# Kernel optimization log

Measured on AMD Instinct MI355X. Metric: run time of the kernel, lower is better.

Reference implementation:

```python
import jax, jax.numpy as jnp
import numpy as np

N, D_IN, H, D_EMB = 2048, 128, 256, 64


def setup_inputs() -> dict:
    key = jax.random.key(0)
    ks = jax.random.split(key, 8)
    x = jax.random.normal(ks[0], (N, D_IN), dtype=jnp.float32)
    adj = jnp.zeros((N, N), dtype=jnp.float32)  # only its last dim is used (eye sizing)
    s = 0.05
    W0 = jax.random.normal(ks[1], (D_IN, H), dtype=jnp.float32) * s
    b0 = jnp.zeros((H,), dtype=jnp.float32)
    W1 = jax.random.normal(ks[2], (H, D_EMB), dtype=jnp.float32) * s
    b1 = jnp.zeros((D_EMB,), dtype=jnp.float32)
    W2 = jax.random.normal(ks[3], (D_IN, D_IN), dtype=jnp.float32) * s
    b2 = jnp.zeros((D_IN,), dtype=jnp.float32)
    temp = jnp.float32(0.1)
    theta = jnp.float32(0.1)
    return {"x": x, "adj": adj, "W0": W0, "b0": b0, "W1": W1, "b1": b1,
            "W2": W2, "b2": b2, "temp": temp, "theta": theta}


def reference(x, adj, W0, b0, W1, b1, W2, b2, temp, theta):
    # layer 0 (on x) and middle layer 1 (on out_x), both with ReLU activation
    out_x = jax.nn.relu(x @ W0 + b0)            # [N, H]
    emb = jax.nn.relu(out_x @ W1 + b1)          # [N, D_EMB]
    # last layer is applied to the ORIGINAL x (per the `x = model(x)` branch)
    x_last = x @ W2 + b2                        # [N, D_IN]

    # dist[i,j] = -||emb_i - emb_j||^2, computed via the gemm expansion
    sq = jnp.sum(emb * emb, axis=1)             # [N]
    dist = -(sq[:, None] + sq[None, :] - 2.0 * (emb @ emb.T))  # [N, N]

    prob = jax.nn.sigmoid((1.0 + temp) * dist + (5.0 + theta))
    A = prob + jnp.eye(adj.shape[-1], dtype=prob.dtype)        # [N, N]

    # diag(A.sum(-1))^{-1} @ A @ x_last  ==  rowwise divide by degree
    deg = jnp.sum(A, axis=-1)                   # [N]
    out = jax.nn.relu((A @ x_last) / deg[:, None])

    # sigmoid(.) > 0 everywhere, so all N*N entries are nonzero: adj_wts is the
    # full flattened adjacency (data-independent shape, jit-safe)
    adj_wts = A.reshape(-1)
    return out, adj_wts
```

## Files before the change

### kernel.cpp

```cpp
#include <hip/hip_runtime.h>
#include <hip/hip_bf16.h>


typedef short bf16x8 __attribute__((ext_vector_type(8)));
typedef float f32x4 __attribute__((ext_vector_type(4)));

__device__ __forceinline__ unsigned short f2bf(float f) {
    unsigned u = __float_as_uint(f);
    unsigned r = u + 0x7fffu + ((u >> 16) & 1u);
    return (unsigned short)(r >> 16);
}

__device__ __forceinline__ bf16x8 pack_bf8(const float* p) {
    union { unsigned u[4]; bf16x8 v; } r;
    #pragma unroll
    for (int i = 0; i < 4; ++i)
        r.u[i] = __builtin_amdgcn_perm(__float_as_uint(p[2 * i + 1]),
                                       __float_as_uint(p[2 * i]), 0x07060302u);
    return r.v;
}

__global__ __launch_bounds__(512) void k1_mlp(
    const float* __restrict__ x,
    const float* __restrict__ W0, const float* __restrict__ b0,
    const float* __restrict__ W1, const float* __restrict__ b1,
    const float* __restrict__ W2, const float* __restrict__ b2,
    unsigned short* __restrict__ emb_bf,
    unsigned short* __restrict__ xlT_bf,
    float* __restrict__ sq,
    float* __restrict__ deg,
    float* __restrict__ outAcc)
{
    __shared__ float xs[8 * 132];
    __shared__ float oxs[8 * 260];
    __shared__ unsigned short xls[128 * 8];
    const int t = threadIdx.x;
    const int r0 = blockIdx.x * 8;

    if (t < 256) {
        int row = t >> 5, c4 = t & 31;
        float4 v = *(const float4*)(x + (r0 + row) * 128 + c4 * 4);
        *(float4*)(&xs[row * 132 + c4 * 4]) = v;
    }
    if (t < 8) deg[r0 + t] = 0.0f;
    *(float2*)(&outAcc[blockIdx.x * 1024 + t * 2]) = make_float2(0.f, 0.f);
    __syncthreads();

    {
        int c = t & 255, rg = t >> 8;
        float bb = b0[c];
        float acc[4] = {bb, bb, bb, bb};
        for (int kk = 0; kk < 32; ++kk) {
            float wa = W0[(kk * 4 + 0) * 256 + c];
            float wb = W0[(kk * 4 + 1) * 256 + c];
            float wc = W0[(kk * 4 + 2) * 256 + c];
            float wd = W0[(kk * 4 + 3) * 256 + c];
            #pragma unroll
            for (int r = 0; r < 4; ++r) {
                float4 xv = *(const float4*)(&xs[(rg * 4 + r) * 132 + kk * 4]);
                acc[r] += xv.x * wa + xv.y * wb + xv.z * wc + xv.w * wd;
            }
        }
        #pragma unroll
        for (int r = 0; r < 4; ++r) oxs[(rg * 4 + r) * 260 + c] = fmaxf(acc[r], 0.0f);
    }
    __syncthreads();

    {
        int h = t & 63, r = t >> 6;
        float acc = b1[h];
        for (int kk = 0; kk < 64; ++kk) {
            float wa = W1[(kk * 4 + 0) * 64 + h];
            float wb = W1[(kk * 4 + 1) * 64 + h];
            float wc = W1[(kk * 4 + 2) * 64 + h];
            float wd = W1[(kk * 4 + 3) * 64 + h];
            float4 xv = *(const float4*)(&oxs[r * 260 + kk * 4]);
            acc += xv.x * wa + xv.y * wb + xv.z * wc + xv.w * wd;
        }
        float e = fmaxf(acc, 0.0f);
        emb_bf[(r0 + r) * 64 + h] = f2bf(e);
        float s = e * e;
        #pragma unroll
        for (int off = 32; off; off >>= 1) s += __shfl_xor(s, off);
        if (h == 0) sq[r0 + r] = s;
    }

    {
        int c = t & 127, rg = t >> 7;
        float bb = b2[c];
        float acc[2] = {bb, bb};
        for (int kk = 0; kk < 32; ++kk) {
            float wa = W2[(kk * 4 + 0) * 128 + c];
            float wb = W2[(kk * 4 + 1) * 128 + c];
            float wc = W2[(kk * 4 + 2) * 128 + c];
            float wd = W2[(kk * 4 + 3) * 128 + c];
            #pragma unroll
            for (int r = 0; r < 2; ++r) {
                float4 xv = *(const float4*)(&xs[(rg * 2 + r) * 132 + kk * 4]);
                acc[r] += xv.x * wa + xv.y * wb + xv.z * wc + xv.w * wd;
            }
        }
        unsigned short p0 = f2bf(acc[0]), p1 = f2bf(acc[1]);
        *(unsigned int*)(&xls[c * 8 + rg * 2]) = (unsigned)p0 | ((unsigned)p1 << 16);
    }
    __syncthreads();
    if (t < 128) {
        uint4 v = *(const uint4*)(&xls[t * 8]);
        *(uint4*)(&xlT_bf[t * 2048 + r0]) = v;
    }
}

__global__ __launch_bounds__(256) void k2f(
    const unsigned short* __restrict__ emb_bf,
    const unsigned short* __restrict__ xlT_bf,
    const float* __restrict__ sq,
    const float* __restrict__ tempp, const float* __restrict__ thetap,
    float* __restrict__ adjw,
    float* __restrict__ outAcc,
    float* __restrict__ deg)
{
    constexpr int LDP = 132;
    __shared__ float Pt[2][16 * LDP];

    const int t = threadIdx.x;
    const int lane = t & 63;
    const int w = t >> 6;
    const int m = lane & 15;
    const int q = lane >> 4;
    const int i0 = blockIdx.x * 16;
    const int jstrip0 = blockIdx.y * 256;
    const float scale = 1.0f + tempp[0];
    const float bias = 5.0f + thetap[0];

    bf16x8 a0 = *(const bf16x8*)(emb_bf + (size_t)(i0 + m) * 64 + q * 8);
    bf16x8 a1 = *(const bf16x8*)(emb_bf + (size_t)(i0 + m) * 64 + 32 + q * 8);
    float sqIr[4];
    #pragma unroll
    for (int r = 0; r < 4; ++r) sqIr[r] = sq[i0 + q * 4 + r];

    f32x4 accO0 = {0.f, 0.f, 0.f, 0.f};
    f32x4 accO1 = {0.f, 0.f, 0.f, 0.f};
    float dega[4] = {0.f, 0.f, 0.f, 0.f};
    const int cg = w * 32;

    #pragma unroll
    for (int jt = 0; jt < 2; ++jt) {
        const int j0 = jstrip0 + jt * 128;
        float* P = &Pt[jt][0];

        #pragma unroll
        for (int s = 0; s < 2; ++s) {
            const int col = (w * 2 + s) * 16 + m;
            const unsigned short* ebj = emb_bf + (size_t)(j0 + col) * 64;
            bf16x8 b0 = *(const bf16x8*)(ebj + q * 8);
            bf16x8 b1 = *(const bf16x8*)(ebj + 32 + q * 8);
            f32x4 S = {0.f, 0.f, 0.f, 0.f};
            S = __builtin_amdgcn_mfma_f32_16x16x32_bf16(a0, b0, S, 0, 0, 0);
            S = __builtin_amdgcn_mfma_f32_16x16x32_bf16(a1, b1, S, 0, 0, 0);

            const float csqJ = sq[j0 + col];
            const int gcol = j0 + col;
            #pragma unroll
            for (int r = 0; r < 4; ++r) {
                int grow = i0 + q * 4 + r;
                float dist = 2.0f * S[r] - sqIr[r] - csqJ;
                float z = scale * dist + bias;
                float p = 1.0f / (1.0f + __expf(-z));
                if (grow == gcol) p += 1.0f;
                dega[r] += p;
                P[(q * 4 + r) * LDP + col] = p;
            }
        }
        __syncthreads();

        {
            int row = t >> 4;
            int c0 = (t & 15) * 8;
            f32x4 v0 = *(const f32x4*)(&P[row * LDP + c0]);
            f32x4 v1 = *(const f32x4*)(&P[row * LDP + c0 + 4]);
            f32x4* dst = (f32x4*)(adjw + (size_t)(i0 + row) * 2048 + j0 + c0);
            __builtin_nontemporal_store(v0, dst);
            __builtin_nontemporal_store(v1, dst + 1);
        }

        #pragma unroll
        for (int s = 0; s < 4; ++s) {
            float af[8];
            *(f32x4*)(&af[0]) = *(const f32x4*)(&P[m * LDP + s * 32 + q * 8]);
            *(f32x4*)(&af[4]) = *(const f32x4*)(&P[m * LDP + s * 32 + q * 8 + 4]);
            bf16x8 aa = pack_bf8(af);
            const int k = j0 + s * 32 + q * 8;
            bf16x8 b0 = *(const bf16x8*)(xlT_bf + (size_t)(cg + m) * 2048 + k);
            bf16x8 b1 = *(const bf16x8*)(xlT_bf + (size_t)(cg + 16 + m) * 2048 + k);
            accO0 = __builtin_amdgcn_mfma_f32_16x16x32_bf16(aa, b0, accO0, 0, 0, 0);
            accO1 = __builtin_amdgcn_mfma_f32_16x16x32_bf16(aa, b1, accO1, 0, 0, 0);
        }
    }

    #pragma unroll
    for (int r = 0; r < 4; ++r) {
        float v = dega[r];
        v += __shfl_xor(v, 1);
        v += __shfl_xor(v, 2);
        v += __shfl_xor(v, 4);
        v += __shfl_xor(v, 8);
        if (m == 0) atomicAdd(&deg[i0 + q * 4 + r], v);
    }
    #pragma unroll
    for (int r = 0; r < 4; ++r) {
        int row = i0 + q * 4 + r;
        atomicAdd(&outAcc[row * 128 + cg + m], accO0[r]);
        atomicAdd(&outAcc[row * 128 + cg + 16 + m], accO1[r]);
    }
}

__global__ __launch_bounds__(256) void k3_fin(float* __restrict__ out,
                                              const float* __restrict__ deg) {
    int idx = blockIdx.x * 1024 + threadIdx.x * 4;
    float4 v = *(float4*)(&out[idx]);
    float dinv = 1.0f / deg[idx >> 7];
    v.x = fmaxf(v.x * dinv, 0.f);
    v.y = fmaxf(v.y * dinv, 0.f);
    v.z = fmaxf(v.z * dinv, 0.f);
    v.w = fmaxf(v.w * dinv, 0.f);
    *(float4*)(&out[idx]) = v;
}

extern "C" void kernel_launch(void* const* d_in, const int* in_sizes, int n_in,
                              void* d_out, int out_size, void* d_ws, size_t ws_size,
                              hipStream_t stream) {
    const float* x     = (const float*)d_in[0];
    const float* W0    = (const float*)d_in[2];
    const float* b0    = (const float*)d_in[3];
    const float* W1    = (const float*)d_in[4];
    const float* b1    = (const float*)d_in[5];
    const float* W2    = (const float*)d_in[6];
    const float* b2    = (const float*)d_in[7];
    const float* temp  = (const float*)d_in[8];
    const float* theta = (const float*)d_in[9];

    char* ws = (char*)d_ws;
    unsigned short* emb_bf = (unsigned short*)(ws);
    unsigned short* xlT_bf = (unsigned short*)(ws + 262144);
    float* sq  = (float*)(ws + 786432);
    float* deg = (float*)(ws + 794624);

    float* outAcc = (float*)d_out;
    float* adjw   = (float*)d_out + 262144;

    k1_mlp<<<256, 512, 0, stream>>>(x, W0, b0, W1, b1, W2, b2,
                                    emb_bf, xlT_bf, sq, deg, outAcc);
    k2f<<<dim3(128, 8), 256, 0, stream>>>(emb_bf, xlT_bf, sq, temp, theta,
                                          adjw, outAcc, deg);
    k3_fin<<<256, 256, 0, stream>>>(outAcc, deg);
}
```

Measured before the change: 126.3 us.

## Use bf16 MFMA for MLP layers and replace atomics with partial-sum reduction

The MLP kernel now computes all three small GEMMs (x@W0, out_x@W1, x@W2) with bf16 16x16x32 MFMA instructions on 16-row blocks instead of scalar FP32 FMAs. The large fused kernel no longer atomically adds into the output and degree buffers. It writes per-strip partial sums to workspace, and the final kernel reduces the 8 partials before dividing and applying ReLU. This removes atomic contention and the zero-initialisation step, at the cost of extra workspace traffic and lower input precision in the MLP.

```diff
diff --git a/kernel.cpp b/kernel.cpp
--- a/kernel.cpp
+++ b/kernel.cpp
@@ -11,6 +11,17 @@
     return (unsigned short)(r >> 16);
 }
 
+__device__ __forceinline__ bf16x8 pack_rne8(const float* p) {
+    union { unsigned u[4]; bf16x8 v; } r;
+    #pragma unroll
+    for (int i = 0; i < 4; ++i) {
+        unsigned lo = __float_as_uint(p[2 * i]) + 0x8000u;
+        unsigned hi = __float_as_uint(p[2 * i + 1]) + 0x8000u;
+        r.u[i] = __builtin_amdgcn_perm(hi, lo, 0x07060302u);
+    }
+    return r.v;
+}
+
 __device__ __forceinline__ bf16x8 pack_bf8(const float* p) {
     union { unsigned u[4]; bf16x8 v; } r;
     #pragma unroll
@@ -20,94 +31,103 @@
     return r.v;
 }
 
-__global__ __launch_bounds__(512) void k1_mlp(
+__global__ __launch_bounds__(256) void k1_mfma(
     const float* __restrict__ x,
     const float* __restrict__ W0, const float* __restrict__ b0,
     const float* __restrict__ W1, const float* __restrict__ b1,
     const float* __restrict__ W2, const float* __restrict__ b2,
     unsigned short* __restrict__ emb_bf,
     unsigned short* __restrict__ xlT_bf,
-    float* __restrict__ sq,
-    float* __restrict__ deg,
-    float* __restrict__ outAcc)
+    float* __restrict__ sq)
 {
-    __shared__ float xs[8 * 132];
-    __shared__ float oxs[8 * 260];
-    __shared__ unsigned short xls[128 * 8];
+    constexpr int LDO = 264;
+    __shared__ unsigned short oxb[16 * LDO];
+    __shared__ float sqs[4][16];
+
     const int t = threadIdx.x;
-    const int r0 = blockIdx.x * 8;
-
-    if (t < 256) {
-        int row = t >> 5, c4 = t & 31;
-        float4 v = *(const float4*)(x + (r0 + row) * 128 + c4 * 4);
-        *(float4*)(&xs[row * 132 + c4 * 4]) = v;
-    }
-    if (t < 8) deg[r0 + t] = 0.0f;
-    *(float2*)(&outAcc[blockIdx.x * 1024 + t * 2]) = make_float2(0.f, 0.f);
+    const int lane = t & 63;
+    const int w = t >> 6;
+    const int m = lane & 15;
+    const int q = lane >> 4;
+    const int i0 = blockIdx.x * 16;
+
+    bf16x8 ax[4];
+    #pragma unroll
+    for (int kb = 0; kb < 4; ++kb) {
+        float xf[8];
+        *(f32x4*)&xf[0] = *(const f32x4*)(x + (size_t)(i0 + m) * 128 + kb * 32 + q * 8);
+        *(f32x4*)&xf[4] = *(const f32x4*)(x + (size_t)(i0 + m) * 128 + kb * 32 + q * 8 + 4);
+        ax[kb] = pack_rne8(xf);
+    }
+
+    #pragma unroll
+    for (int hh = 0; hh < 4; ++hh) {
+        const int h = (w * 4 + hh) * 16 + m;
+        float bb = b0[h];
+        f32x4 acc = {bb, bb, bb, bb};
+        #pragma unroll
+        for (int kb = 0; kb < 4; ++kb) {
+            float wf[8];
+            #pragma unroll
+            for (int j = 0; j < 8; ++j) wf[j] = W0[(size_t)(kb * 32 + q * 8 + j) * 256 + h];
+            acc = __builtin_amdgcn_mfma_f32_16x16x32_bf16(ax[kb], pack_rne8(wf), acc, 0, 0, 0);
+        }
+        #pragma unroll
+        for (int r = 0; r < 4; ++r)
+            oxb[(q * 4 + r) * LDO + h] = f2bf(fmaxf(acc[r], 0.0f));
+    }
     __syncthreads();
 
     {
-        int c = t & 255, rg = t >> 8;
-        float bb = b0[c];
-        float acc[4] = {bb, bb, bb, bb};
-        for (int kk = 0; kk < 32; ++kk) {
-            float wa = W0[(kk * 4 + 0) * 256 + c];
-            float wb = W0[(kk * 4 + 1) * 256 + c];
-            float wc = W0[(kk * 4 + 2) * 256 + c];
-            float wd = W0[(kk * 4 + 3) * 256 + c];
-            #pragma unroll
-            for (int r = 0; r < 4; ++r) {
-                float4 xv = *(const float4*)(&xs[(rg * 4 + r) * 132 + kk * 4]);
-                acc[r] += xv.x * wa + xv.y * wb + xv.z * wc + xv.w * wd;
-            }
-        }
-        #pragma unroll
-        for (int r = 0; r < 4; ++r) oxs[(rg * 4 + r) * 260 + c] = fmaxf(acc[r], 0.0f);
+        const int h = w * 16 + m;
+        float bb = b1[h];
+        f32x4 acc = {bb, bb, bb, bb};
+        #pragma unroll
+        for (int kb = 0; kb < 8; ++kb) {
+            bf16x8 af = *(const bf16x8*)(&oxb[m * LDO + kb * 32 + q * 8]);
+            float wf[8];
+            #pragma unroll
+            for (int j = 0; j < 8; ++j) wf[j] = W1[(size_t)(kb * 32 + q * 8 + j) * 64 + h];
+            acc = __builtin_amdgcn_mfma_f32_16x16x32_bf16(af, pack_rne8(wf), acc, 0, 0, 0);
+        }
+        float s2[4];
+        #pragma unroll
+        for (int r = 0; r < 4; ++r) {
+            float e = fmaxf(acc[r], 0.0f);
+            emb_bf[(size_t)(i0 + q * 4 + r) * 64 + h] = f2bf(e);
+            s2[r] = e * e;
+        }
+        #pragma unroll
+        for (int r = 0; r < 4; ++r) {
+            float v = s2[r];
+            v += __shfl_xor(v, 1);
+            v += __shfl_xor(v, 2);
+            v += __shfl_xor(v, 4);
+            v += __shfl_xor(v, 8);
+            if (m == 0) sqs[w][q * 4 + r] = v;
+        }
+    }
+
+    #pragma unroll
+    for (int hh = 0; hh < 2; ++hh) {
+        const int c = (w * 2 + hh) * 16 + m;
+        float bb = b2[c];
+        f32x4 acc = {bb, bb, bb, bb};
+        #pragma unroll
+        for (int kb = 0; kb < 4; ++kb) {
+            float wf[8];
+            #pragma unroll
+            for (int j = 0; j < 8; ++j) wf[j] = W2[(size_t)(kb * 32 + q * 8 + j) * 128 + c];
+            acc = __builtin_amdgcn_mfma_f32_16x16x32_bf16(ax[kb], pack_rne8(wf), acc, 0, 0, 0);
+        }
+        uint2 pk;
+        pk.x = (unsigned)f2bf(acc[0]) | ((unsigned)f2bf(acc[1]) << 16);
+        pk.y = (unsigned)f2bf(acc[2]) | ((unsigned)f2bf(acc[3]) << 16);
+        *(uint2*)(&xlT_bf[(size_t)c * 2048 + i0 + q * 4]) = pk;
     }
     __syncthreads();
-
-    {
-        int h = t & 63, r = t >> 6;
-        float acc = b1[h];
-        for (int kk = 0; kk < 64; ++kk) {
-            float wa = W1[(kk * 4 + 0) * 64 + h];
-            float wb = W1[(kk * 4 + 1) * 64 + h];
-            float wc = W1[(kk * 4 + 2) * 64 + h];
-            float wd = W1[(kk * 4 + 3) * 64 + h];
-            float4 xv = *(const float4*)(&oxs[r * 260 + kk * 4]);
-            acc += xv.x * wa + xv.y * wb + xv.z * wc + xv.w * wd;
-        }
-        float e = fmaxf(acc, 0.0f);
-        emb_bf[(r0 + r) * 64 + h] = f2bf(e);
-        float s = e * e;
-        #pragma unroll
-        for (int off = 32; off; off >>= 1) s += __shfl_xor(s, off);
-        if (h == 0) sq[r0 + r] = s;
-    }
-
-    {
-        int c = t & 127, rg = t >> 7;
-        float bb = b2[c];
-        float acc[2] = {bb, bb};
-        for (int kk = 0; kk < 32; ++kk) {
-            float wa = W2[(kk * 4 + 0) * 128 + c];
-            float wb = W2[(kk * 4 + 1) * 128 + c];
-            float wc = W2[(kk * 4 + 2) * 128 + c];
-            float wd = W2[(kk * 4 + 3) * 128 + c];
-            #pragma unroll
-            for (int r = 0; r < 2; ++r) {
-                float4 xv = *(const float4*)(&xs[(rg * 2 + r) * 132 + kk * 4]);
-                acc[r] += xv.x * wa + xv.y * wb + xv.z * wc + xv.w * wd;
-            }
-        }
-        unsigned short p0 = f2bf(acc[0]), p1 = f2bf(acc[1]);
-        *(unsigned int*)(&xls[c * 8 + rg * 2]) = (unsigned)p0 | ((unsigned)p1 << 16);
-    }
-    __syncthreads();
-    if (t < 128) {
-        uint4 v = *(const uint4*)(&xls[t * 8]);
-        *(uint4*)(&xlT_bf[t * 2048 + r0]) = v;
-    }
+    if (t < 16)
+        sq[i0 + t] = sqs[0][t] + sqs[1][t] + sqs[2][t] + sqs[3][t];
 }
 
 __global__ __launch_bounds__(256) void k2f(
@@ -116,11 +136,12 @@
     const float* __restrict__ sq,
     const float* __restrict__ tempp, const float* __restrict__ thetap,
     float* __restrict__ adjw,
-    float* __restrict__ outAcc,
-    float* __restrict__ deg)
+    float* __restrict__ outPart,
+    float* __restrict__ degPart)
 {
     constexpr int LDP = 132;
     __shared__ float Pt[2][16 * LDP];
+    __shared__ float degS[4][16];
 
     const int t = threadIdx.x;
     const int lane = t & 63;
@@ -128,7 +149,8 @@
     const int m = lane & 15;
     const int q = lane >> 4;
     const int i0 = blockIdx.x * 16;
-    const int jstrip0 = blockIdx.y * 256;
+    const int bj = blockIdx.y;
+    const int jstrip0 = bj * 256;
     const float scale = 1.0f + tempp[0];
     const float bias = 5.0f + thetap[0];
 
@@ -204,26 +226,41 @@
         v += __shfl_xor(v, 2);
         v += __shfl_xor(v, 4);
         v += __shfl_xor(v, 8);
-        if (m == 0) atomicAdd(&deg[i0 + q * 4 + r], v);
-    }
+        if (m == 0) degS[w][q * 4 + r] = v;
+    }
+    __syncthreads();
+    if (t < 16)
+        degPart[bj * 2048 + i0 + t] =
+            degS[0][t] + degS[1][t] + degS[2][t] + degS[3][t];
+
+    float* op = outPart + ((size_t)bj * 2048 + i0) * 128;
     #pragma unroll
     for (int r = 0; r < 4; ++r) {
-        int row = i0 + q * 4 + r;
-        atomicAdd(&outAcc[row * 128 + cg + m], accO0[r]);
-        atomicAdd(&outAcc[row * 128 + cg + 16 + m], accO1[r]);
-    }
-}
-
-__global__ __launch_bounds__(256) void k3_fin(float* __restrict__ out,
-                                              const float* __restrict__ deg) {
-    int idx = blockIdx.x * 1024 + threadIdx.x * 4;
-    float4 v = *(float4*)(&out[idx]);
-    float dinv = 1.0f / deg[idx >> 7];
-    v.x = fmaxf(v.x * dinv, 0.f);
-    v.y = fmaxf(v.y * dinv, 0.f);
-    v.z = fmaxf(v.z * dinv, 0.f);
-    v.w = fmaxf(v.w * dinv, 0.f);
-    *(float4*)(&out[idx]) = v;
+        op[(q * 4 + r) * 128 + cg + m] = accO0[r];
+        op[(q * 4 + r) * 128 + cg + 16 + m] = accO1[r];
+    }
+}
+
+__global__ __launch_bounds__(256) void k3_fin(
+    const float* __restrict__ outPart, const float* __restrict__ degPart,
+    float* __restrict__ out)
+{
+    int idx4 = (blockIdx.x * 256 + threadIdx.x) * 4;
+    int row = idx4 >> 7;
+    float4 s = make_float4(0.f, 0.f, 0.f, 0.f);
+    float d = 0.f;
+    #pragma unroll
+    for (int p = 0; p < 8; ++p) {
+        float4 v = *(const float4*)(&outPart[(size_t)p * 262144 + idx4]);
+        s.x += v.x; s.y += v.y; s.z += v.z; s.w += v.w;
+        d += degPart[p * 2048 + row];
+    }
+    float dinv = 1.0f / d;
+    s.x = fmaxf(s.x * dinv, 0.f);
+    s.y = fmaxf(s.y * dinv, 0.f);
+    s.z = fmaxf(s.z * dinv, 0.f);
+    s.w = fmaxf(s.w * dinv, 0.f);
+    *(float4*)(&out[idx4]) = s;
 }
 
 extern "C" void kernel_launch(void* const* d_in, const int* in_sizes, int n_in,
@@ -242,15 +279,16 @@
     char* ws = (char*)d_ws;
     unsigned short* emb_bf = (unsigned short*)(ws);
     unsigned short* xlT_bf = (unsigned short*)(ws + 262144);
-    float* sq  = (float*)(ws + 786432);
-    float* deg = (float*)(ws + 794624);
-
-    float* outAcc = (float*)d_out;
-    float* adjw   = (float*)d_out + 262144;
-
-    k1_mlp<<<256, 512, 0, stream>>>(x, W0, b0, W1, b1, W2, b2,
-                                    emb_bf, xlT_bf, sq, deg, outAcc);
+    float* sq      = (float*)(ws + 786432);
+    float* degPart = (float*)(ws + 794624);
+    float* outPart = (float*)(ws + 860160);
+
+    float* out  = (float*)d_out;
+    float* adjw = (float*)d_out + 262144;
+
+    k1_mfma<<<128, 256, 0, stream>>>(x, W0, b0, W1, b1, W2, b2,
+                                     emb_bf, xlT_bf, sq);
     k2f<<<dim3(128, 8), 256, 0, stream>>>(emb_bf, xlT_bf, sq, temp, theta,
-                                          adjw, outAcc, deg);
-    k3_fin<<<256, 256, 0, stream>>>(outAcc, deg);
-}
+                                          adjw, outPart, degPart);
+    k3_fin<<<256, 256, 0, stream>>>(outPart, degPart, out);
+}
```

Result: faster. 113.4 us (-10.2%).
